# Kernel tuning notes

Hardware: AMD Instinct MI355X
Metric: run time of the kernel (lower is better)

Reference implementation:

```python
import jax, jax.numpy as jnp
import numpy as np

EPS = 1e-5
LEAK = 0.01  # PADLoC uses ABN = BatchNorm + LeakyReLU as norm_act


def bn_act(x, g, b):
    # train-mode batch norm over (B,H,W) + leaky relu
    mu = jnp.mean(x, axis=(0, 2, 3), keepdims=True)
    var = jnp.var(x, axis=(0, 2, 3), keepdims=True)
    y = (x - mu) * jax.lax.rsqrt(var + EPS) * g[None, :, None, None] + b[None, :, None, None]
    return jnp.where(y >= 0, y, LEAK * y)


def depthwise3x3(x, w):
    # x: (B,C,H,W), w: (C,1,3,3), dilation (1,1), padding 1, groups=C
    C = x.shape[1]
    return jax.lax.conv_general_dilated(
        x, w, window_strides=(1, 1), padding=((1, 1), (1, 1)),
        feature_group_count=C, dimension_numbers=('NCHW', 'OIHW', 'NCHW'))


def pointwise(x, w):
    # 1x1 conv, no bias; w: (Cout, Cin)
    return jnp.einsum('bchw,oc->bohw', x, w)


def _gather_vals(x_flat, idx):
    # x_flat: (B,C,P), idx: (B,HW,9) float indices -> (B,C,HW,9)
    B, C, P = x_flat.shape
    i = idx.astype(jnp.int32).reshape(B, -1)  # (B, HW*9)
    out = jax.vmap(lambda xf, ii: xf[:, ii])(x_flat, i)  # (B,C,HW*9)
    return out.reshape(B, C, idx.shape[1], 9)


def setup_inputs() -> dict:
    key = jax.random.key(0)
    ks = jax.random.split(key, 8)
    B, Cin, Cout, H, W = 1, 256, 128, 64, 192
    sc = 0.05
    return {
        'x': jax.random.normal(ks[0], (B, Cin, H, W), jnp.float32),
        'x_range': jax.random.normal(ks[1], (B, 1, H, W), jnp.float32),
        'range_out': jax.random.normal(ks[2], (Cin, 1, 3, 3), jnp.float32) * sc,
        'w_reduce': jax.random.normal(ks[3], (Cout, Cin), jnp.float32) * sc,
        'g_r': jnp.ones((Cout,), jnp.float32), 'b_r': jnp.zeros((Cout,), jnp.float32),
        'dw1': jax.random.normal(ks[4], (Cout, 1, 3, 3), jnp.float32) * sc,
        'pw1': jax.random.normal(ks[5], (Cout, Cout), jnp.float32) * sc,
        'g1': jnp.ones((Cout,), jnp.float32), 'b1': jnp.zeros((Cout,), jnp.float32),
        'dw2': jax.random.normal(ks[6], (Cout, 1, 3, 3), jnp.float32) * sc,
        'pw2': jax.random.normal(ks[7], (Cout, Cout), jnp.float32) * sc,
        'g2': jnp.ones((Cout,), jnp.float32), 'b2': jnp.zeros((Cout,), jnp.float32),
    }


def reference(x, x_range, range_out, w_reduce, g_r, b_r, dw1, pw1, g1, b1, dw2, pw2, g2, b2):
    B, Cin, H, W = x.shape
    Hp, Wp = H + 2, W + 2
    P = Hp * Wp  # flattened padded spatial size
    x_off = jnp.array([-1, 0, 1, -1, 0, 1, -1, 0, 1], jnp.float32)
    y_off = jnp.array([-1, -1, -1, 0, 0, 0, 1, 1, 1], jnp.float32)

    offset = 3.0 * jax.nn.sigmoid(x_range)  # (B,1,H,W)

    # base (undeformed) flattened indices of the 9 taps around each interior pixel
    v = jnp.arange(P, dtype=jnp.float32)[:, None]  # (P,1)
    pre_v = v + x_off + y_off * Wp                 # (P,9)
    pre_v = pre_v.reshape(Hp, Wp, 9)[1:H + 1, 1:W + 1].reshape(-1, 9)  # (HW,9)
    pre_v = jnp.broadcast_to(pre_v[None], (B, H * W, 9))

    # fractional offsets: only x-direction is scaled by offset in _3x3box
    offset_v = offset.reshape(B, H * W, 1) * x_off.reshape(1, 1, 9) + (y_off * Wp).reshape(1, 1, 9)

    x_padded = jnp.pad(x, ((0, 0), (0, 0), (1, 1), (1, 1)))  # (B,C,Hp,Wp)
    clamp = lambda a: jnp.clip(a, 0.0, P - 1.0)

    after_v = pre_v + offset_v
    av_f = clamp(pre_v + jnp.floor(offset_v))
    av_f1 = clamp(av_f + x_off)
    av_c = clamp(pre_v + jnp.ceil(offset_v))
    av_c1 = clamp(av_c + x_off)

    xflat = x_padded.reshape(B, Cin, P)
    vf = _gather_vals(xflat, av_f)
    vf1 = _gather_vals(xflat, av_f1)
    vc = _gather_vals(xflat, av_c)
    vc1 = _gather_vals(xflat, av_c1)

    f1 = jnp.abs(after_v - av_f)[:, None] * vf + jnp.abs(av_f1 - after_v)[:, None] * vf1
    f2 = jnp.abs(after_v - av_c1)[:, None] * vc1 + jnp.abs(av_c - after_v)[:, None] * vc
    interp = (jnp.abs((after_v - av_f) / Wp)[:, None] * f1
              + jnp.abs((av_c1 - after_v) / Wp)[:, None] * f2)  # (B,C,HW,9)

    y = jnp.sum(interp * range_out.reshape(1, Cin, 1, 9), -1).reshape(B, Cin, H, W)
    y = bn_act(pointwise(y, w_reduce), g_r, b_r)
    y = bn_act(pointwise(depthwise3x3(y, dw1), pw1), g1, b1)
    y = bn_act(pointwise(depthwise3x3(y, dw2), pw2), g2, b2)
    return y
```

## Files before the change

### kernel.cpp

```cpp
#include <hip/hip_runtime.h>

#define HW    12288
#define Wimg  192
#define Himg  64
#define Wpad  194
#define Ppad  12804

typedef __attribute__((ext_vector_type(8))) __bf16 bf16x8;
typedef __attribute__((ext_vector_type(4))) float  f32x4;

static __device__ __forceinline__ unsigned short f2bf(float f) {
    union { float f; unsigned int u; } v; v.f = f;
    unsigned int r = v.u + 0x7fffu + ((v.u >> 16) & 1u);
    return (unsigned short)(r >> 16);
}
static __device__ __forceinline__ float bf2f(unsigned short h) {
    union { unsigned int u; float f; } v; v.u = ((unsigned int)h) << 16;
    return v.f;
}
static __device__ __forceinline__ float bflo(unsigned int u) {
    union { unsigned int u; float f; } v; v.u = u << 16; return v.f;
}
static __device__ __forceinline__ float bfhi(unsigned int u) {
    union { unsigned int u; float f; } v; v.u = u & 0xffff0000u; return v.f;
}

__global__ __launch_bounds__(256, 6) void k_deform(
    const float* __restrict__ x,
    const float* __restrict__ xr,
    const float* __restrict__ rout,
    unsigned short* __restrict__ y0,
    const float* __restrict__ wr,
    const float* __restrict__ pw1,
    const float* __restrict__ pw2,
    unsigned short* __restrict__ W1h, unsigned short* __restrict__ W1l,
    unsigned short* __restrict__ W2h, unsigned short* __restrict__ W2l,
    unsigned short* __restrict__ W3h, unsigned short* __restrict__ W3l)
{
    __shared__ unsigned short s_x[32][240];

    const int cblk = blockIdx.x;
    const int tile = blockIdx.y;
    const int tid  = threadIdx.x;

    if (tile == 192) {
        const int base = cblk * 256 + tid;
        #pragma unroll
        for (int k = 0; k < 32; ++k) {
            const int idx = base + k * 2048;
            float v;
            unsigned short *dh, *dl;
            if (idx < 32768)      { v = wr[idx];         dh = W1h + idx; dl = W1l + idx; }
            else if (idx < 49152) { int u = idx - 32768; v = pw1[u]; dh = W2h + u; dl = W2l + u; }
            else                  { int u = idx - 49152; v = pw2[u]; dh = W3h + u; dl = W3l + u; }
            unsigned short hh = f2bf(v);
            *dh = hh;
            *dl = f2bf(v - bf2f(hh));
        }
        return;
    }

    const int pl   = tid & 63;
    const int wv   = __builtin_amdgcn_readfirstlane(tid >> 6);
    const int h    = tile / 3;
    const int w0   = (tile - h * 3) * 64;
    const int w    = w0 + pl;
    const int gp   = h * Wimg + w;

    int   li[6];
    float gw[6][3];
    const float off = 3.0f / (1.0f + expf(-xr[gp]));

    #pragma unroll
    for (int t = 0; t < 6; ++t) {
        const int xo = (t & 1) ? 1 : -1;
        const int yo = (t >> 1) - 1;
        float ov  = off * (float)xo;
        int   iv  = yo * Wpad;
        int   pre = (h + 1) * Wpad + (w + 1) + xo + iv;
        float after = (float)(pre + iv) + ov;
        int fl = (int)floorf(ov);
        int ce = (int)ceilf(ov);
        int av_f  = min(max(pre + fl + iv, 0), Ppad - 1);
        int av_f1 = min(max(av_f + xo,    0), Ppad - 1);
        int av_c  = min(max(pre + ce + iv, 0), Ppad - 1);
        int av_c1 = min(max(av_c + xo,    0), Ppad - 1);
        float wf  = fabsf(after - (float)av_f);
        float wf1 = fabsf((float)av_f1 - after);
        float wc1 = fabsf(after - (float)av_c1);
        float wc  = fabsf((float)av_c - after);
        float s1 = wf  * (1.0f / Wpad);
        float s2 = wc1 * (1.0f / Wpad);
        int   i4[4] = { av_f, av_f1, av_c1, av_c };
        float w4[4] = { s1 * wf, s1 * wf1, s2 * wc1, s2 * wc };
        int b = min(min(i4[0], i4[1]), min(i4[2], i4[3]));
        const int base = (h + 1 + 2 * yo) * Wpad + w0 - 4;
        li[t] = (t >> 1) * 80 + min(max(b - base, 0), 71);
        #pragma unroll
        for (int s = 0; s < 3; ++s) {
            float ws = 0.0f;
            #pragma unroll
            for (int j = 0; j < 4; ++j)
                ws += (i4[j] == b + s) ? w4[j] : 0.0f;
            int av = b + s;
            int r  = av / Wpad;
            int cc = av - r * Wpad;
            bool inb = (r >= 1) && (r <= Himg) && (cc >= 1) && (cc <= Wimg);
            gw[t][s] = inb ? ws : 0.0f;
        }
    }

    const int jj = tid;
    int  xoff = 0;
    bool valid = false;
    int  rr = 0, jcol = 0;
    if (jj < 222) {
        rr   = jj / 74;
        jcol = jj - rr * 74;
        const int flat = (h + 1 + 2 * (rr - 1)) * Wpad + w0 - 4 + jcol;
        if (flat >= 0 && flat < Ppad) {
            const int r = flat / Wpad;
            const int c = flat - r * Wpad;
            valid = (r >= 1) && (r <= Himg) && (c >= 1) && (c <= Wimg);
            xoff  = valid ? ((r - 1) * Wimg + (c - 1)) : 0;
        }
    }
    const float* xb = x + (size_t)(cblk * 32) * HW;
    for (int c = 0; c < 32; ++c) {
        if (jj < 222) {
            float v = valid ? xb[(size_t)c * HW + xoff] : 0.0f;
            s_x[c][rr * 80 + jcol] = f2bf(v);
        }
    }
    __syncthreads();

    const int c0l = wv * 8;
    #pragma unroll 2
    for (int i = 0; i < 8; ++i) {
        const int cl = c0l + i;
        const unsigned short* sxc = s_x[cl];
        const float* rc = rout + (cblk * 32 + cl) * 9;
        float acc = 0.0f;
        #pragma unroll
        for (int t = 0; t < 6; ++t) {
            float part = gw[t][0] * bf2f(sxc[li[t]])
                       + gw[t][1] * bf2f(sxc[li[t] + 1])
                       + gw[t][2] * bf2f(sxc[li[t] + 2]);
            const int k = 3 * (t >> 1) + ((t & 1) ? 2 : 0);
            acc += rc[k] * part;
        }
        y0[(size_t)(cblk * 32 + cl) * HW + gp] = f2bf(acc);
    }
}

template <int CIN>
__global__ __launch_bounds__(256, 4) void k_pw_mfma(
    const unsigned short* __restrict__ Aact,
    const unsigned short* __restrict__ Whi,
    const unsigned short* __restrict__ Wlo,
    unsigned short* __restrict__ Z,
    float* __restrict__ part)
{
    constexpr int KC = CIN / 32;
    constexpr int RS = CIN + 8;
    __shared__ __align__(16) unsigned short s_b[32][RS];

    const int tid = threadIdx.x;
    const int l   = tid & 63;
    const int wv  = tid >> 6;
    const int px0 = blockIdx.x * 32;
    const int o0  = blockIdx.y * 64;

    {
        const int cs  = tid >> 1;
        const int pxb = (tid & 1) << 4;
        const int swz = (tid & 1) << 3;
        #pragma unroll
        for (int it = 0; it < CIN / 128; ++it) {
            const int c = cs + it * 128;
            const uint4* src = (const uint4*)(Aact + (size_t)c * HW + px0 + pxb);
            uint4 u0 = src[0];
            uint4 u1 = src[1];
            const int sc = c ^ swz;
            unsigned int wd[8] = {u0.x, u0.y, u0.z, u0.w, u1.x, u1.y, u1.z, u1.w};
            #pragma unroll
            for (int e = 0; e < 8; ++e) {
                s_b[pxb + 2 * e    ][sc] = (unsigned short)(wd[e] & 0xffffu);
                s_b[pxb + 2 * e + 1][sc] = (unsigned short)(wd[e] >> 16);
            }
        }
    }

    const int orow = o0 + wv * 16 + (l & 15);
    const unsigned short* whp = Whi + (size_t)orow * CIN + ((l >> 4) << 3);
    const unsigned short* wlp = Wlo + (size_t)orow * CIN + ((l >> 4) << 3);
    bf16x8 wh[KC], wl[KC];
    #pragma unroll
    for (int kc = 0; kc < KC; ++kc) {
        wh[kc] = *(const bf16x8*)(whp + kc * 32);
        wl[kc] = *(const bf16x8*)(wlp + kc * 32);
    }

    __syncthreads();

    f32x4 acc[2] = { {0.f, 0.f, 0.f, 0.f}, {0.f, 0.f, 0.f, 0.f} };
    const int prow = l & 15;
    const int kg8  = l >> 4;
    #pragma unroll
    for (int kc = 0; kc < KC; ++kc) {
        #pragma unroll
        for (int ip = 0; ip < 2; ++ip) {
            const int col = kc * 32 + (((kg8 ^ ip) & 3) << 3);
            bf16x8 bfr = *(const bf16x8*)&s_b[ip * 16 + prow][col];
            acc[ip] = __builtin_amdgcn_mfma_f32_16x16x32_bf16(wh[kc], bfr, acc[ip], 0, 0, 0);
            acc[ip] = __builtin_amdgcn_mfma_f32_16x16x32_bf16(wl[kc], bfr, acc[ip], 0, 0, 0);
        }
    }

    float* pp = part + (size_t)blockIdx.x * 256;
    const int obase = o0 + wv * 16 + ((l >> 4) << 2);
    #pragma unroll
    for (int r = 0; r < 4; ++r) {
        const int ch = obase + r;
        float v0 = acc[0][r];
        float v1 = acc[1][r];
        Z[(size_t)ch * HW + px0 + prow]      = f2bf(v0);
        Z[(size_t)ch * HW + px0 + 16 + prow] = f2bf(v1);
        float s = v0 + v1;
        float q = v0 * v0 + v1 * v1;
        s += __shfl_xor(s, 1, 64);  q += __shfl_xor(q, 1, 64);
        s += __shfl_xor(s, 2, 64);  q += __shfl_xor(q, 2, 64);
        s += __shfl_xor(s, 4, 64);  q += __shfl_xor(q, 4, 64);
        s += __shfl_xor(s, 8, 64);  q += __shfl_xor(q, 8, 64);
        if (prow == 0) {
            pp[2 * ch]     = s;
            pp[2 * ch + 1] = q;
        }
    }
}

__global__ __launch_bounds__(256) void k_dw(
    const unsigned short* __restrict__ Zs,
    const float* __restrict__ part,
    const float* __restrict__ g,
    const float* __restrict__ b,
    const float* __restrict__ dwgt,
    ushort4* __restrict__ D)
{
    __shared__ float rs[4], rq[4];
    __shared__ __align__(16) unsigned short s_z[9 * 200 + 8];
    const int tid = threadIdx.x;
    const int bx  = blockIdx.x;
    const int c   = bx / 12;
    const int m   = bx - c * 12;
    const int g0  = m * 1024;
    const int r0  = g0 / Wimg;

    const unsigned short* zc = Zs + (size_t)c * HW;
    if (tid < 216) {
        const int rr = tid / 24;
        const int cc = (tid - rr * 24) * 8;
        const int gr = r0 - 1 + rr;
        uint4 u = make_uint4(0u, 0u, 0u, 0u);
        if (gr >= 0 && gr < Himg)
            u = *(const uint4*)(zc + (size_t)gr * Wimg + cc);
        *(uint4*)&s_z[rr * 200 + 8 + cc] = u;
    } else if (tid < 226) {
        *(uint4*)&s_z[(tid - 216) * 200] = make_uint4(0u, 0u, 0u, 0u);
    }

    float s = 0.0f, q = 0.0f;
    for (int bb = tid; bb < 384; bb += 256) {
        const float* pb = part + (size_t)bb * 256 + 2 * c;
        s += pb[0];
        q += pb[1];
    }
    #pragma unroll
    for (int off = 32; off > 0; off >>= 1) {
        s += __shfl_down(s, off, 64);
        q += __shfl_down(q, off, 64);
    }
    if ((tid & 63) == 0) { rs[tid >> 6] = s; rq[tid >> 6] = q; }
    __syncthreads();
    s = rs[0] + rs[1] + rs[2] + rs[3];
    q = rq[0] + rq[1] + rq[2] + rq[3];

    const float mu  = s * (1.0f / HW);
    const float var = q * (1.0f / HW) - mu * mu;
    const float sc  = g[c] * rsqrtf(var + 1e-5f);
    const float sh  = b[c] - mu * sc;

    float wk[9];
    #pragma unroll
    for (int k = 0; k < 9; ++k) wk[k] = dwgt[c * 9 + k];

    const int gg = g0 + tid * 4;
    const int h  = gg / Wimg;
    const int w0 = gg - h * Wimg;
    const int lr = h - (r0 - 1);

    float v[3][6];
    #pragma unroll
    for (int ky = 0; ky < 3; ++ky) {
        const int hh  = h + ky - 1;
        const bool rin = (hh >= 0) && (hh < Himg);
        const unsigned short* sr = &s_z[(lr - 1 + ky) * 200 + 7 + w0];
        #pragma unroll
        for (int j = 0; j < 6; ++j) {
            const int ww = w0 - 1 + j;
            const bool in = rin && (ww >= 0) && (ww < Wimg);
            float z = bf2f(sr[j]);
            float y = z * sc + sh;
            y = (y >= 0.0f) ? y : 0.01f * y;
            v[ky][j] = in ? y : 0.0f;
        }
    }

    ushort4 o;
    float oo[4];
    #pragma unroll
    for (int j = 0; j < 4; ++j) {
        float a = 0.0f;
        #pragma unroll
        for (int ky = 0; ky < 3; ++ky)
            #pragma unroll
            for (int kx = 0; kx < 3; ++kx)
                a += wk[ky * 3 + kx] * v[ky][j + kx];
        oo[j] = a;
    }
    o.x = f2bf(oo[0]); o.y = f2bf(oo[1]); o.z = f2bf(oo[2]); o.w = f2bf(oo[3]);
    D[bx * 256 + tid] = o;
}

__global__ __launch_bounds__(256) void k_final(
    const unsigned short* __restrict__ Zs,
    const float* __restrict__ part,
    const float* __restrict__ g,
    const float* __restrict__ b,
    float4* __restrict__ out)
{
    __shared__ float rs[4], rq[4];
    const int tid = threadIdx.x;
    const int c   = blockIdx.x / 12;

    float s = 0.0f, q = 0.0f;
    for (int bb = tid; bb < 384; bb += 256) {
        const float* pb = part + (size_t)bb * 256 + 2 * c;
        s += pb[0];
        q += pb[1];
    }
    #pragma unroll
    for (int off = 32; off > 0; off >>= 1) {
        s += __shfl_down(s, off, 64);
        q += __shfl_down(q, off, 64);
    }
    if ((tid & 63) == 0) { rs[tid >> 6] = s; rq[tid >> 6] = q; }
    __syncthreads();
    s = rs[0] + rs[1] + rs[2] + rs[3];
    q = rq[0] + rq[1] + rq[2] + rq[3];

    const float mu  = s * (1.0f / HW);
    const float var = q * (1.0f / HW) - mu * mu;
    const float sc  = g[c] * rsqrtf(var + 1e-5f);
    const float sh  = b[c] - mu * sc;

    const int f = blockIdx.x * 256 + tid;
    uint2 a = ((const uint2*)Zs)[f];
    float4 v;
    v.x = bflo(a.x) * sc + sh; v.x = (v.x >= 0.0f) ? v.x : 0.01f * v.x;
    v.y = bfhi(a.x) * sc + sh; v.y = (v.y >= 0.0f) ? v.y : 0.01f * v.y;
    v.z = bflo(a.y) * sc + sh; v.z = (v.z >= 0.0f) ? v.z : 0.01f * v.z;
    v.w = bfhi(a.y) * sc + sh; v.w = (v.w >= 0.0f) ? v.w : 0.01f * v.w;
    out[f] = v;
}

extern "C" void kernel_launch(void* const* d_in, const int* in_sizes, int n_in,
                              void* d_out, int out_size, void* d_ws, size_t ws_size,
                              hipStream_t stream) {
    const float* x   = (const float*)d_in[0];
    const float* xr  = (const float*)d_in[1];
    const float* ro  = (const float*)d_in[2];
    const float* wr  = (const float*)d_in[3];
    const float* gr  = (const float*)d_in[4];
    const float* br  = (const float*)d_in[5];
    const float* dw1 = (const float*)d_in[6];
    const float* pw1 = (const float*)d_in[7];
    const float* g1  = (const float*)d_in[8];
    const float* b1  = (const float*)d_in[9];
    const float* dw2 = (const float*)d_in[10];
    const float* pw2 = (const float*)d_in[11];
    const float* g2  = (const float*)d_in[12];
    const float* b2  = (const float*)d_in[13];

    unsigned short* WS = (unsigned short*)d_ws;
    unsigned short* y0 = WS;
    unsigned short* Z1 = WS + 3145728;
    unsigned short* D  = WS + 4718592;
    unsigned short* Z2 = WS + 6291456;
    unsigned short* Z3 = WS + 7864320;
    unsigned short* W1h = WS + 9438720;
    unsigned short* W1l = WS + 9471488;
    unsigned short* W2h = WS + 9504256;
    unsigned short* W2l = WS + 9520640;
    unsigned short* W3h = WS + 9537024;
    unsigned short* W3l = WS + 9553408;
    float* part1 = (float*)(WS + 6291456);
    float* part2 = (float*)WS;
    float* part3 = (float*)WS;
    float* out = (float*)d_out;

    k_deform<<<dim3(8, 193), 256, 0, stream>>>(x, xr, ro, y0, wr, pw1, pw2,
                                               W1h, W1l, W2h, W2l, W3h, W3l);
    k_pw_mfma<256><<<dim3(384, 2), 256, 0, stream>>>(y0, W1h, W1l, Z1, part1);
    k_dw<<<1536, 256, 0, stream>>>(Z1, part1, gr, br, dw1, (ushort4*)D);
    k_pw_mfma<128><<<dim3(384, 2), 256, 0, stream>>>(D, W2h, W2l, Z2, part2);
    k_dw<<<1536, 256, 0, stream>>>(Z2, part2, g1, b1, dw2, (ushort4*)D);
    k_pw_mfma<128><<<dim3(384, 2), 256, 0, stream>>>(D, W3h, W3l, Z3, part3);
    k_final<<<1536, 256, 0, stream>>>(Z3, part3, g2, b2, (float4*)out);
}
```

Before: 146.8 us.

## Transpose deform shared tile to position-major with vectorized 8-channel loads

The shared-memory staging tile in the deformable gather kernel is changed from channel-major to position-major, padded to a 40-channel stride. Each thread now packs 8 channels into a single 128-bit LDS store, and the interpolation reads 8 channels per tap with one uint4 load. The aim is to cut the number of LDS instructions and bank-conflicted scalar 16-bit accesses. In exchange it uses more registers for eight accumulators and issues all global loads per channel block up front.

```diff
diff --git a/kernel.cpp b/kernel.cpp
--- a/kernel.cpp
+++ b/kernel.cpp
@@ -37,7 +37,7 @@
     unsigned short* __restrict__ W2h, unsigned short* __restrict__ W2l,
     unsigned short* __restrict__ W3h, unsigned short* __restrict__ W3l)
 {
-    __shared__ unsigned short s_x[32][240];
+    __shared__ __align__(16) unsigned short s_x[240 * 40];
 
     const int cblk = blockIdx.x;
     const int tile = blockIdx.y;
@@ -126,31 +126,55 @@
         }
     }
     const float* xb = x + (size_t)(cblk * 32) * HW;
-    for (int c = 0; c < 32; ++c) {
-        if (jj < 222) {
-            float v = valid ? xb[(size_t)c * HW + xoff] : 0.0f;
-            s_x[c][rr * 80 + jcol] = f2bf(v);
+    if (jj < 222) {
+        const int pos = rr * 80 + jcol;
+        #pragma unroll
+        for (int cb = 0; cb < 4; ++cb) {
+            unsigned short tq[8];
+            #pragma unroll
+            for (int i = 0; i < 8; ++i) {
+                float v = valid ? xb[(size_t)(cb * 8 + i) * HW + xoff] : 0.0f;
+                tq[i] = f2bf(v);
+            }
+            uint4 u;
+            u.x = (unsigned)tq[0] | ((unsigned)tq[1] << 16);
+            u.y = (unsigned)tq[2] | ((unsigned)tq[3] << 16);
+            u.z = (unsigned)tq[4] | ((unsigned)tq[5] << 16);
+            u.w = (unsigned)tq[6] | ((unsigned)tq[7] << 16);
+            *(uint4*)&s_x[pos * 40 + cb * 8] = u;
         }
     }
     __syncthreads();
 
-    const int c0l = wv * 8;
-    #pragma unroll 2
-    for (int i = 0; i < 8; ++i) {
-        const int cl = c0l + i;
-        const unsigned short* sxc = s_x[cl];
-        const float* rc = rout + (cblk * 32 + cl) * 9;
-        float acc = 0.0f;
-        #pragma unroll
-        for (int t = 0; t < 6; ++t) {
-            float part = gw[t][0] * bf2f(sxc[li[t]])
-                       + gw[t][1] * bf2f(sxc[li[t] + 1])
-                       + gw[t][2] * bf2f(sxc[li[t] + 2]);
-            const int k = 3 * (t >> 1) + ((t & 1) ? 2 : 0);
-            acc += rc[k] * part;
-        }
-        y0[(size_t)(cblk * 32 + cl) * HW + gp] = f2bf(acc);
-    }
+    const int c0l  = wv * 8;
+    const int cb16 = wv << 3;
+    float acc[8] = {0.f,0.f,0.f,0.f,0.f,0.f,0.f,0.f};
+    #pragma unroll
+    for (int t = 0; t < 6; ++t) {
+        const int k = 3 * (t >> 1) + ((t & 1) ? 2 : 0);
+        float part[8];
+        #pragma unroll
+        for (int s = 0; s < 3; ++s) {
+            uint4 u = *(const uint4*)&s_x[(li[t] + s) * 40 + cb16];
+            const float g = gw[t][s];
+            float v0 = bflo(u.x), v1 = bfhi(u.x), v2 = bflo(u.y), v3 = bfhi(u.y);
+            float v4 = bflo(u.z), v5 = bfhi(u.z), v6 = bflo(u.w), v7 = bfhi(u.w);
+            if (s == 0) {
+                part[0] = g * v0; part[1] = g * v1; part[2] = g * v2; part[3] = g * v3;
+                part[4] = g * v4; part[5] = g * v5; part[6] = g * v6; part[7] = g * v7;
+            } else {
+                part[0] += g * v0; part[1] += g * v1; part[2] += g * v2; part[3] += g * v3;
+                part[4] += g * v4; part[5] += g * v5; part[6] += g * v6; part[7] += g * v7;
+            }
+        }
+        const float* rc = rout + (size_t)(cblk * 32 + c0l) * 9 + k;
+        #pragma unroll
+        for (int i = 0; i < 8; ++i)
+            acc[i] += rc[i * 9] * part[i];
+    }
+    #pragma unroll
+    for (int i = 0; i < 8; ++i)
+        y0[(size_t)(cblk * 32 + c0l + i) * HW + gp] = f2bf(acc[i]);
 }
 
 template <int CIN>
```

New measurement: 148.2 us. No clear change (+0.9%).
